# Kernel optimization log

Hardware: AMD Instinct MI355X
Metric: run time of the kernel (lower is better)

## Reference

```python
import jax, jax.numpy as jnp
import numpy as np
import math

NUM_HEADS = 16
HEAVY_RATIO = 0.1
RECENT_RATIO = 0.1
ROPE_THETA = 10000.0


def setup_inputs() -> dict:
    key = jax.random.key(0)
    ks = jax.random.split(key, 5)
    b, s, h = 1, 2048, 2048
    return {
        "hidden_states": jax.random.normal(ks[0], (b, s, h), dtype=jnp.float32),
        "Wq": jax.random.normal(ks[1], (h, h), dtype=jnp.float32) * 0.02,
        "Wk": jax.random.normal(ks[2], (h, h), dtype=jnp.float32) * 0.02,
        "Wv": jax.random.normal(ks[3], (h, h), dtype=jnp.float32) * 0.02,
        "Wo": jax.random.normal(ks[4], (h, h), dtype=jnp.float32) * 0.02,
    }


def _rotate_half(x):
    d = x.shape[-1]
    return jnp.concatenate([-x[..., d // 2:], x[..., : d // 2]], axis=-1)


def _rope(q, k, seq_len, head_dim, dtype):
    # LLaMA rotary embedding: inv_freq over even dims, emb = [freqs, freqs]
    inv_freq = 1.0 / (ROPE_THETA ** (jnp.arange(0, head_dim, 2, dtype=jnp.float32) / head_dim))
    pos = jnp.arange(seq_len, dtype=jnp.float32)
    freqs = pos[:, None] * inv_freq[None, :]            # [s, d/2]
    emb = jnp.concatenate([freqs, freqs], axis=-1)       # [s, d]
    cos = jnp.cos(emb).astype(dtype)[None, None]         # [1,1,s,d]
    sin = jnp.sin(emb).astype(dtype)[None, None]
    q = q * cos + _rotate_half(q) * sin
    k = k * cos + _rotate_half(k) * sin
    return q, k


def reference(hidden_states, Wq, Wk, Wv, Wo):
    b, s, hidden = hidden_states.shape
    H = NUM_HEADS
    d = hidden // H

    def proj(W):  # nn.Linear(x) = x @ W.T, then split heads -> [b,H,s,d]
        return (hidden_states @ W.T).reshape(b, s, H, d).transpose(0, 2, 1, 3)

    q, k, v = proj(Wq), proj(Wk), proj(Wv)
    q, k = _rope(q, k, s, d, hidden_states.dtype)

    scores = jnp.einsum("bhqd,bhkd->bhqk", q, k) / math.sqrt(d)  # [b,H,s,s]
    neg = jnp.finfo(scores.dtype).min
    i = jnp.arange(s)[:, None]
    j = jnp.arange(s)[None, :]
    causal = jnp.where(j <= i, jnp.array(0.0, scores.dtype), neg)
    scores = jnp.maximum(scores + causal, neg)

    heavy_budget = int(HEAVY_RATIO * s)
    recent_budget = int(RECENT_RATIO * s)

    # first softmax (fp32), accumulate column importances
    tmp_attn = jax.nn.softmax(scores.astype(jnp.float32), axis=-1).astype(scores.dtype)
    tmp_sum = jnp.sum(tmp_attn, axis=-2)                 # [b,H,s]
    _, topk_idx = jax.lax.top_k(tmp_sum, heavy_budget)   # [b,H,heavy]
    heavy_mask = jnp.any(topk_idx[..., :, None] == jnp.arange(s)[None, None, None, :], axis=-2)  # [b,H,s]

    # recent band: tril(diag=recent) & triu(diag=-recent)  <=>  |i-j| <= recent
    band = jnp.abs(i - j) <= recent_budget               # [s,s]
    mask = heavy_mask[:, :, None, :] | band[None, None]

    scores = jnp.where(mask, scores, neg)
    probs = jax.nn.softmax(scores.astype(jnp.float32), axis=-1).astype(q.dtype)
    attn = jnp.einsum("bhqk,bhkd->bhqd", probs, v)
    attn = attn.transpose(0, 2, 1, 3).reshape(b, s, hidden)
    return attn @ Wo.T
```

## Files before the change

### kernel.cpp

```cpp
#include <hip/hip_runtime.h>
#include <hip/hip_bf16.h>
#include <stdint.h>

#define SEQ   2048
#define HIDN  2048
#define NHEAD 16
#define HDIM  128
#define HEAVY 204
#define RECENT 204

typedef __attribute__((ext_vector_type(4))) float f32x4;
typedef __attribute__((ext_vector_type(8))) short bf16x8;
typedef unsigned short u16;
typedef unsigned int   u32;

static __device__ __forceinline__ u16 f2bf(float f){
  union { float f; u32 u; } v; v.f = f;
  u32 r = (v.u + 0x7FFFu + ((v.u >> 16) & 1u)) >> 16;
  return (u16)r;
}
static __device__ __forceinline__ float bf2f(u16 u){
  union { u32 u; float f; } v; v.u = ((u32)u) << 16;
  return v.f;
}

static __device__ __forceinline__ void gload16(const void* g, void* l){
  __builtin_amdgcn_global_load_lds((const __attribute__((address_space(1))) u32*)g,
                                   (__attribute__((address_space(3))) u32*)l, 16, 0, 0);
}

#define WAITVM(N) asm volatile("s_waitcnt vmcnt(" #N ")" ::: "memory")
#define BARRAW    __builtin_amdgcn_s_barrier()
#define PRIO1     __builtin_amdgcn_s_setprio(1)
#define PRIO0     __builtin_amdgcn_s_setprio(0)

static __device__ __forceinline__ void stage_tile(const u16* __restrict__ base, size_t stride,
                                                  int row0, u16* __restrict__ lds, int tid){
  const int wbase = tid & ~63;
#pragma unroll
  for (int it = 0; it < 4; ++it){
    int m = it * 256 + tid;
    int row = m >> 4, cp = m & 15;
    gload16(base + (size_t)(row0 + row) * stride + ((cp ^ (row & 7)) * 8),
            lds + (it * 256 + wbase) * 8);
  }
}

static __device__ __forceinline__ void stageK512(const u16* __restrict__ base, size_t stride,
                                                 int row0, u16* __restrict__ lds, int tid){
#pragma unroll
  for (int it = 0; it < 2; ++it){
    int m = it * 512 + tid;
    int row = m >> 4, cp = m & 15;
    gload16(base + (size_t)(row0 + row) * stride + ((cp ^ (row & 7)) * 8),
            lds + (it * 512 + (tid & ~63)) * 8);
  }
}
static __device__ __forceinline__ void stageV512(const u16* __restrict__ base, size_t stride,
                                                 int c0, u16* __restrict__ lds, int tid){
#pragma unroll
  for (int it = 0; it < 2; ++it){
    int m = it * 512 + tid;
    int row = m >> 3, cp = m & 7;
    gload16(base + (size_t)row * stride + c0 + ((cp ^ (row & 7)) * 8),
            lds + (it * 512 + (tid & ~63)) * 8);
  }
}

__global__ void k_prep(const float* __restrict__ A0, const float* __restrict__ A1,
                       const float* __restrict__ A2, const float* __restrict__ A3,
                       const float* __restrict__ A4, u16* __restrict__ out,
                       float* __restrict__ cosT, float* __restrict__ sinT,
                       float* __restrict__ colsum){
  int b = blockIdx.x, tid = threadIdx.x;
  if (b < 20480){
    int id = b * 256 + tid;
    int sel = id >> 20, off = (id & 1048575) * 4;
    const float* src = sel == 0 ? A0 : sel == 1 ? A1 : sel == 2 ? A2 : sel == 3 ? A3 : A4;
    float4 v = *(const float4*)(src + off);
    ushort4 o;
    o.x = f2bf(v.x); o.y = f2bf(v.y); o.z = f2bf(v.z); o.w = f2bf(v.w);
    *(ushort4*)(out + (size_t)sel * 4194304 + off) = o;
  } else if (b < 20992){
    int i = (b - 20480) * 256 + tid;
    int pos = i >> 6, j = i & 63;
    float invf = powf(10000.0f, -(float)j * (1.0f / 64.0f));
    float a = (float)pos * invf;
    cosT[i] = cosf(a);
    sinT[i] = sinf(a);
  } else {
    int i = (b - 20992) * 256 + tid;
    if (i < 16384) ((float4*)colsum)[i] = (float4){0.f, 0.f, 0.f, 0.f};
  }
}

__global__ void k_post(u16* __restrict__ Qm, u16* __restrict__ Km,
                       const float* __restrict__ cosT, const float* __restrict__ sinT,
                       const u16* __restrict__ V, u16* __restrict__ Vt){
  __shared__ u16 t[32][33];
  int b = blockIdx.x, tid = threadIdx.x;
  if (b < 4096){
    int gid = b * 256 + tid;
    u16* M = (gid < 524288) ? Qm : Km;
    int id = gid & 524287;
    int pos = id >> 8, rem = id & 255;
    int h = rem >> 4, j4 = (rem & 15) * 4;
    u16* p = M + (size_t)pos * HIDN + h * HDIM + j4;
    ushort4 lo = *(ushort4*)p;
    ushort4 hi = *(ushort4*)(p + 64);
    float4 c = *(const float4*)(cosT + pos * 64 + j4);
    float4 s = *(const float4*)(sinT + pos * 64 + j4);
    float l0 = bf2f(lo.x), l1 = bf2f(lo.y), l2 = bf2f(lo.z), l3 = bf2f(lo.w);
    float h0 = bf2f(hi.x), h1 = bf2f(hi.y), h2 = bf2f(hi.z), h3 = bf2f(hi.w);
    ushort4 nlo, nhi;
    nlo.x = f2bf(l0 * c.x - h0 * s.x);  nhi.x = f2bf(h0 * c.x + l0 * s.x);
    nlo.y = f2bf(l1 * c.y - h1 * s.y);  nhi.y = f2bf(h1 * c.y + l1 * s.y);
    nlo.z = f2bf(l2 * c.z - h2 * s.z);  nhi.z = f2bf(h2 * c.z + l2 * s.z);
    nlo.w = f2bf(l3 * c.w - h3 * s.w);  nhi.w = f2bf(h3 * c.w + l3 * s.w);
    *(ushort4*)p = nlo;
    *(ushort4*)(p + 64) = nhi;
  } else {
    int b2 = b - 4096;
    int s0 = (b2 & 63) * 32, c0 = (b2 >> 6) * 32;
    int r = tid >> 3, cc = (tid & 7) * 4;
    ushort4 v = *(const ushort4*)(V + (size_t)(s0 + r) * 2048 + c0 + cc);
    t[r][cc] = v.x; t[r][cc + 1] = v.y; t[r][cc + 2] = v.z; t[r][cc + 3] = v.w;
    __syncthreads();
    int co = tid >> 3, ro = (tid & 7) * 4;
    ushort4 o;
    o.x = t[ro][co]; o.y = t[ro + 1][co]; o.z = t[ro + 2][co]; o.w = t[ro + 3][co];
    *(ushort4*)(Vt + (size_t)(c0 + co) * 2048 + s0 + ro) = o;
  }
}

__global__ __launch_bounds__(512, 1)
void k_g256(const u16* __restrict__ X, const u16* __restrict__ Wq, const u16* __restrict__ Wk,
            const u16* __restrict__ Wv, u16* __restrict__ C0, u16* __restrict__ C1,
            u16* __restrict__ C2){
  __shared__ __align__(16) u16 LA[2][256 * 64];
  __shared__ __align__(16) u16 LB[2][192 * 64];
  const int tid = threadIdx.x;
  const int lane = tid & 63, wvi = tid >> 6;
  const int wm = wvi >> 2, wn = wvi & 3;
  const int g = lane >> 4, c15 = lane & 15;
  const int brow = blockIdx.y * 256;
  const int bcol = blockIdx.x * 192;
  const int NT = 32;

  f32x4 acc[8][3];
#pragma unroll
  for (int m = 0; m < 8; m++)
#pragma unroll
    for (int n = 0; n < 3; n++) acc[m][n] = (f32x4){0.f, 0.f, 0.f, 0.f};

  const int cc0 = ((g ^ (c15 & 7)) * 8);
  bf16x8 af[4][2], af2[4][2], bf[3][2];

#define BPTR(rB_) (rB_ < 2048 ? Wq + (size_t)(rB_) * 2048 \
                 : rB_ < 4096 ? Wk + (size_t)((rB_) - 2048) * 2048 \
                              : Wv + (size_t)((rB_) - 4096) * 2048)
#define STGA(grow0, gcol0, ldsb) do { \
  _Pragma("unroll") for (int it = 0; it < 2; ++it){ \
    int m_ = it * 512 + tid; \
    int row_ = m_ >> 3, cp_ = m_ & 7; \
    gload16(X + (size_t)((grow0) + row_) * 2048 + (gcol0) + ((cp_ ^ (row_ & 7)) * 8), \
            (ldsb) + (it * 512 + (tid & ~63)) * 8); \
  } } while(0)
#define STGB128(gcol0, ldsb) do { \
  _Pragma("unroll") for (int it = 0; it < 2; ++it){ \
    int m_ = it * 512 + tid; \
    int row_ = m_ >> 3, cp_ = m_ & 7; \
    int rB_ = bcol + row_; \
    const u16* bp_ = BPTR(rB_); \
    gload16(bp_ + (gcol0) + ((cp_ ^ (row_ & 7)) * 8), \
            (ldsb) + (it * 512 + (tid & ~63)) * 8); \
  } } while(0)
#define STGB64(gcol0, ldsb) do { \
    int row_ = 128 + (tid >> 3), cp_ = tid & 7; \
    int rB_ = bcol + row_; \
    const u16* bp_ = BPTR(rB_); \
    gload16(bp_ + (gcol0) + ((cp_ ^ (row_ & 7)) * 8), \
            (ldsb) + (tid & ~63) * 8); \
  } while(0)
#define RDA(buf) \
  _Pragma("unroll") for (int mi2 = 0; mi2 < 4; ++mi2){ \
    const u16* pr = &LA[buf][0] + (size_t)(wm * 128 + mi2 * 16 + c15) * 64; \
    af[mi2][0] = *(const bf16x8*)(pr + cc0); \
    af[mi2][1] = *(const bf16x8*)(pr + (cc0 ^ 32)); \
  }
#define RDA2(buf) \
  _Pragma("unroll") for (int mi2 = 0; mi2 < 4; ++mi2){ \
    const u16* pr = &LA[buf][0] + (size_t)(wm * 128 + (4 + mi2) * 16 + c15) * 64; \
    af2[mi2][0] = *(const bf16x8*)(pr + cc0); \
    af2[mi2][1] = *(const bf16x8*)(pr + (cc0 ^ 32)); \
  }
#define RDB2(buf) \
  _Pragma("unroll") for (int ni2 = 0; ni2 < 2; ++ni2){ \
    const u16* pr = &LB[buf][0] + (size_t)(wn * 48 + ni2 * 16 + c15) * 64; \
    bf[ni2][0] = *(const bf16x8*)(pr + cc0); \
    bf[ni2][1] = *(const bf16x8*)(pr + (cc0 ^ 32)); \
  }
#define RDB1(buf) do { \
    const u16* pr = &LB[buf][0] + (size_t)(wn * 48 + 32 + c15) * 64; \
    bf[2][0] = *(const bf16x8*)(pr + cc0); \
    bf[2][1] = *(const bf16x8*)(pr + (cc0 ^ 32)); \
  } while(0)
#define MM2A \
  _Pragma("unroll") for (int mi2 = 0; mi2 < 4; ++mi2) \
  _Pragma("unroll") for (int ni2 = 0; ni2 < 2; ++ni2) \
  _Pragma("unroll") for (int kk = 0; kk < 2; ++kk) \
    acc[mi2][ni2] = __builtin_amdgcn_mfma_f32_16x16x32_bf16( \
        af[mi2][kk], bf[ni2][kk], acc[mi2][ni2], 0, 0, 0);
#define MM1AB \
  _Pragma("unroll") for (int mi2 = 0; mi2 < 4; ++mi2) \
  _Pragma("unroll") for (int kk = 0; kk < 2; ++kk){ \
    acc[mi2][2] = __builtin_amdgcn_mfma_f32_16x16x32_bf16( \
        af[mi2][kk], bf[2][kk], acc[mi2][2], 0, 0, 0); \
    acc[4 + mi2][2] = __builtin_amdgcn_mfma_f32_16x16x32_bf16( \
        af2[mi2][kk], bf[2][kk], acc[4 + mi2][2], 0, 0, 0); \
  }
#define MM2B \
  _Pragma("unroll") for (int mi2 = 0; mi2 < 4; ++mi2) \
  _Pragma("unroll") for (int ni2 = 0; ni2 < 2; ++ni2) \
  _Pragma("unroll") for (int kk = 0; kk < 2; ++kk) \
    acc[4 + mi2][ni2] = __builtin_amdgcn_mfma_f32_16x16x32_bf16( \
        af2[mi2][kk], bf[ni2][kk], acc[4 + mi2][ni2], 0, 0, 0);

#define TILE(t, buf) do { \
    const int kn1 = ((t) + 1) * 64; \
    const int kn2 = ((t) + 2) * 64; \
     \
    RDA(buf); RDB2(buf); \
    if ((t) + 1 < NT) STGA(brow, kn1, &LA[buf ^ 1][0]); \
    BARRAW; PRIO1; MM2A; PRIO0; BARRAW; \
     \
    RDB1(buf); RDA2(buf); \
    if ((t) + 1 < NT) STGA(brow + 128, kn1, &LA[buf ^ 1][0] + 128 * 64); \
    BARRAW; PRIO1; MM1AB; PRIO0; BARRAW; \
     \
    if ((t) + 2 < NT){ STGB128(kn2, &LB[buf][0]); STGB64(kn2, &LB[buf][0] + 128 * 64); \
                       WAITVM(3); } \
    else             { WAITVM(0); } \
    BARRAW; PRIO1; MM2B; PRIO0; BARRAW; \
  } while(0)

  STGA(brow,       0, &LA[0][0]);
  STGA(brow + 128, 0, &LA[0][0] + 128 * 64);
  STGB128(0,  &LB[0][0]);
  STGB64(0,   &LB[0][0] + 128 * 64);
  STGB128(64, &LB[1][0]);
  STGB64(64,  &LB[1][0] + 128 * 64);
  WAITVM(3);
  BARRAW;

  for (int t = 0; t < NT; t += 2){
    TILE(t, 0);
    TILE(t + 1, 1);
  }
#undef TILE
#undef BPTR
#undef STGA
#undef STGB128
#undef STGB64
#undef RDA
#undef RDA2
#undef RDB2
#undef RDB1
#undef MM2A
#undef MM1AB
#undef MM2B

#pragma unroll
  for (int mi = 0; mi < 8; ++mi)
#pragma unroll
    for (int ni = 0; ni < 3; ++ni){
      int colbase = bcol + wn * 48 + ni * 16;
      int proj = colbase >> 11;
      u16* Cb = proj == 0 ? C0 : proj == 1 ? C1 : C2;
      int lc = (colbase & 2047) + c15;
#pragma unroll
      for (int r = 0; r < 4; ++r){
        int row = brow + wm * 128 + mi * 16 + g * 4 + r;
        Cb[(size_t)row * 2048 + lc] = f2bf(acc[mi][ni][r]);
      }
    }
}

__global__ __launch_bounds__(512)
void k_gemm_out(const u16* __restrict__ A, const u16* __restrict__ B, float* __restrict__ C){
  __shared__ __align__(16) u16 As[2][128 * 64];
  __shared__ __align__(16) u16 Bs[2][128 * 64];
  const int tid = threadIdx.x;
  const int w = tid >> 6, lane = tid & 63;
  const int wm = w >> 1, wn = w & 1;
  const int g = lane >> 4, c15 = lane & 15;
  const int brow = blockIdx.y * 128, bcol = blockIdx.x * 128;
  const int cc0 = ((g ^ (c15 & 7)) * 8);

  f32x4 acc[2][4];
#pragma unroll
  for (int m = 0; m < 2; m++)
#pragma unroll
    for (int n = 0; n < 4; n++) acc[m][n] = (f32x4){0.f, 0.f, 0.f, 0.f};

#define STG_O(k0, buf) do { \
  _Pragma("unroll") for (int it = 0; it < 2; ++it){ \
    int m_ = it * 512 + tid; \
    int row_ = m_ >> 3, cp_ = m_ & 7; \
    gload16(A + (size_t)(brow + row_) * 2048 + (k0) + ((cp_ ^ (row_ & 7)) * 8), \
            As[buf] + (it * 512 + (tid & ~63)) * 8); \
    gload16(B + (size_t)(bcol + row_) * 2048 + (k0) + ((cp_ ^ (row_ & 7)) * 8), \
            Bs[buf] + (it * 512 + (tid & ~63)) * 8); \
  } } while(0)

  STG_O(0, 0);
  int cur = 0;
  for (int kt = 0; kt < 32; ++kt){
    if (kt + 1 < 32){ STG_O((kt + 1) * 64, cur ^ 1); WAITVM(4); }
    else            { WAITVM(0); }
    BARRAW;
    bf16x8 af[2][2], bfr[4][2];
#pragma unroll
    for (int mi = 0; mi < 2; ++mi){
      const u16* pr = As[cur] + (size_t)(wm * 32 + mi * 16 + c15) * 64;
      af[mi][0] = *(const bf16x8*)(pr + cc0);
      af[mi][1] = *(const bf16x8*)(pr + (cc0 ^ 32));
    }
#pragma unroll
    for (int ni = 0; ni < 4; ++ni){
      const u16* pr = Bs[cur] + (size_t)(wn * 64 + ni * 16 + c15) * 64;
      bfr[ni][0] = *(const bf16x8*)(pr + cc0);
      bfr[ni][1] = *(const bf16x8*)(pr + (cc0 ^ 32));
    }
    PRIO1;
#pragma unroll
    for (int mi = 0; mi < 2; ++mi)
#pragma unroll
      for (int ni = 0; ni < 4; ++ni)
#pragma unroll
        for (int kk = 0; kk < 2; ++kk)
          acc[mi][ni] = __builtin_amdgcn_mfma_f32_16x16x32_bf16(af[mi][kk], bfr[ni][kk],
                                                                acc[mi][ni], 0, 0, 0);
    PRIO0;
    BARRAW;
    cur ^= 1;
  }
#undef STG_O
#pragma unroll
  for (int mi = 0; mi < 2; ++mi)
#pragma unroll
    for (int ni = 0; ni < 4; ++ni)
#pragma unroll
      for (int r = 0; r < 4; ++r){
        int row = brow + wm * 32 + mi * 16 + g * 4 + r;
        int col = bcol + wn * 64 + ni * 16 + c15;
        C[(size_t)row * 2048 + col] = acc[mi][ni][r];
      }
}

__global__ __launch_bounds__(256)
void k_pass1a(const u16* __restrict__ Q, const u16* __restrict__ K, float* __restrict__ rowsum){
  __shared__ __align__(16) u16 Ks[2][64 * 128];
  const int tid = threadIdx.x;
  const int wv = tid >> 6, lane = tid & 63;
  const int g = lane >> 4, c15 = lane & 15;
  const int h = blockIdx.y;
  int qb = 0, c = 0;
  { int rem = blockIdx.x; int q = 0;
    while (rem >= ((2 * q + 9) >> 3)){ rem -= (2 * q + 9) >> 3; q++; }
    qb = q; c = rem; }
  const int i0 = qb * 128;
  const int ktend = 2 * qb + 2;
  const int kt0 = c * 8;
  const int kt1 = (ktend < kt0 + 8) ? ktend : (kt0 + 8);
  const u16* Qh = Q + h * HDIM;
  const u16* Kh = K + h * HDIM;
  const float scale = 0.08838834764831845f;
  const int wb = wv * 32;

  bf16x8 qfr[2][4];
#pragma unroll
  for (int m = 0; m < 2; m++)
#pragma unroll
    for (int ks = 0; ks < 4; ks++)
      qfr[m][ks] = *(const bf16x8*)(Qh + (size_t)(i0 + wb + m * 16 + c15) * 2048 + ks * 32 + g * 8);

  stage_tile(Kh, 2048, kt0 * 64, Ks[0], tid);

  float rs[2][4] = {{0.f,0.f,0.f,0.f},{0.f,0.f,0.f,0.f}};
  int cur = 0;
  for (int kt = kt0; kt < kt1; ++kt){
    if (kt + 1 < kt1){ stage_tile(Kh, 2048, (kt + 1) * 64, Ks[cur ^ 1], tid); WAITVM(4); }
    else             { WAITVM(0); }
    BARRAW;
    const int k0 = kt * 64;
    f32x4 sacc[2][4];
#pragma unroll
    for (int m = 0; m < 2; m++)
#pragma unroll
      for (int n = 0; n < 4; n++) sacc[m][n] = (f32x4){0.f, 0.f, 0.f, 0.f};
#pragma unroll
    for (int ks = 0; ks < 4; ++ks){
#pragma unroll
      for (int n = 0; n < 4; n++){
        int brw = n * 16 + c15;
        bf16x8 b = *(const bf16x8*)(Ks[cur] + brw * 128 + ((ks * 32 + g * 8) ^ ((brw & 7) << 3)));
#pragma unroll
        for (int m = 0; m < 2; m++)
          sacc[m][n] = __builtin_amdgcn_mfma_f32_16x16x32_bf16(qfr[m][ks], b, sacc[m][n], 0, 0, 0);
      }
    }
    if (kt < 2 * qb){
#pragma unroll
      for (int m = 0; m < 2; m++)
#pragma unroll
        for (int n = 0; n < 4; n++)
#pragma unroll
          for (int r = 0; r < 4; r++)
            rs[m][r] += __expf(sacc[m][n][r] * scale);
    } else {
#pragma unroll
      for (int n = 0; n < 4; n++){
        int col = k0 + n * 16 + c15;
#pragma unroll
        for (int m = 0; m < 2; m++)
#pragma unroll
          for (int r = 0; r < 4; r++){
            int rowg = i0 + wb + m * 16 + g * 4 + r;
            rs[m][r] += (col <= rowg) ? __expf(sacc[m][n][r] * scale) : 0.f;
          }
      }
    }
    BARRAW;
    cur ^= 1;
  }
#pragma unroll
  for (int m = 0; m < 2; m++)
#pragma unroll
    for (int r = 0; r < 4; r++){
      float v = rs[m][r];
      v += __shfl_xor(v, 1); v += __shfl_xor(v, 2);
      v += __shfl_xor(v, 4); v += __shfl_xor(v, 8);
      if (c15 == 0)
        atomicAdd(&rowsum[h * 2048 + i0 + wb + m * 16 + g * 4 + r], v);
    }
}

__global__ __launch_bounds__(256)
void k_pass1b(const u16* __restrict__ Q, const u16* __restrict__ K,
              const float* __restrict__ rowsum, float* __restrict__ colsum){
  __shared__ __align__(16) u16 Qs[2][64 * 128];
  const int tid = threadIdx.x;
  const int wv = tid >> 6, lane = tid & 63;
  const int g = lane >> 4, c15 = lane & 15;
  const int h = blockIdx.y;
  int kb = 0, c = 0;
  { int rem = blockIdx.x; int q = 0;
    while (rem >= ((39 - 2 * q) >> 3)){ rem -= (39 - 2 * q) >> 3; q++; }
    kb = q; c = rem; }
  const int k0 = kb * 128;
  const int qt0 = 2 * kb + c * 8;
  const int qt1 = (2 * kb + c * 8 + 8 < 32) ? (2 * kb + c * 8 + 8) : 32;
  const u16* Qh = Q + h * HDIM;
  const u16* Kh = K + h * HDIM;
  const float scale = 0.08838834764831845f;
  const int wb = wv * 32;
  const float* rsrow = rowsum + h * 2048;

  bf16x8 kfr[2][4];
#pragma unroll
  for (int m = 0; m < 2; m++)
#pragma unroll
    for (int ks = 0; ks < 4; ks++)
      kfr[m][ks] = *(const bf16x8*)(Kh + (size_t)(k0 + wb + m * 16 + c15) * 2048 + ks * 32 + g * 8);

  stage_tile(Qh, 2048, qt0 * 64, Qs[0], tid);

  float racc[2][4] = {{0.f,0.f,0.f,0.f},{0.f,0.f,0.f,0.f}};
  int cur = 0;
  for (int qt = qt0; qt < qt1; ++qt){
    if (qt + 1 < qt1){ stage_tile(Qh, 2048, (qt + 1) * 64, Qs[cur ^ 1], tid); WAITVM(4); }
    else             { WAITVM(0); }
    BARRAW;
    const int i0q = qt * 64;
    float rw[4];
#pragma unroll
    for (int n = 0; n < 4; n++)
      rw[n] = 1.0f / rsrow[i0q + n * 16 + c15];
    f32x4 sacc[2][4];
#pragma unroll
    for (int m = 0; m < 2; m++)
#pragma unroll
      for (int n = 0; n < 4; n++) sacc[m][n] = (f32x4){0.f, 0.f, 0.f, 0.f};
#pragma unroll
    for (int ks = 0; ks < 4; ++ks){
#pragma unroll
      for (int n = 0; n < 4; n++){
        int brw = n * 16 + c15;
        bf16x8 b = *(const bf16x8*)(Qs[cur] + brw * 128 + ((ks * 32 + g * 8) ^ ((brw & 7) << 3)));
#pragma unroll
        for (int m = 0; m < 2; m++)
          sacc[m][n] = __builtin_amdgcn_mfma_f32_16x16x32_bf16(kfr[m][ks], b, sacc[m][n], 0, 0, 0);
      }
    }
    if (qt >= 2 * kb + 2){
#pragma unroll
      for (int m = 0; m < 2; m++)
#pragma unroll
        for (int n = 0; n < 4; n++)
#pragma unroll
          for (int r = 0; r < 4; r++)
            racc[m][r] += __expf(sacc[m][n][r] * scale) * rw[n];
    } else {
#pragma unroll
      for (int n = 0; n < 4; n++){
        int colq = i0q + n * 16 + c15;
#pragma unroll
        for (int m = 0; m < 2; m++)
#pragma unroll
          for (int r = 0; r < 4; r++){
            int rowk = k0 + wb + m * 16 + g * 4 + r;
            racc[m][r] += (rowk <= colq) ? __expf(sacc[m][n][r] * scale) * rw[n] : 0.f;
          }
      }
    }
    BARRAW;
    cur ^= 1;
  }
#pragma unroll
  for (int m = 0; m < 2; m++)
#pragma unroll
    for (int r = 0; r < 4; r++){
      float v = racc[m][r];
      v += __shfl_xor(v, 1); v += __shfl_xor(v, 2);
      v += __shfl_xor(v, 4); v += __shfl_xor(v, 8);
      if (c15 == 0)
        atomicAdd(&colsum[h * 2048 + k0 + wb + m * 16 + g * 4 + r], v);
    }
}

__global__ __launch_bounds__(1024)
void k_topk(const float* __restrict__ colsum, short* __restrict__ cidx){
  __shared__ u32 keys[2048];
  __shared__ int hist[256];
  __shared__ int chunkCnt[32];
  __shared__ short cidL[256];
  __shared__ u32 Tacc_s;
  __shared__ int rem_s;
  const int tid = threadIdx.x;
  const int h = blockIdx.x;
  const int w = tid >> 6, lane = tid & 63;

  for (int i = tid; i < 2048; i += 1024) keys[i] = ((const u32*)colsum)[h * 2048 + i];
  if (tid == 0){ Tacc_s = 0; rem_s = HEAVY; }
  __syncthreads();

  for (int s = 24; s >= 0; s -= 8){
    if (tid < 256) hist[tid] = 0;
    __syncthreads();
    u32 T = Tacc_s;
    for (int i = tid; i < 2048; i += 1024){
      u32 k = keys[i];
      bool match = (s == 24) ? true : (((k ^ T) >> (s + 8)) == 0);
      if (match) atomicAdd(&hist[(k >> s) & 255], 1);
    }
    __syncthreads();
    if (tid == 0){
      int rem = rem_s, acc = 0, b = 255;
      for (; b > 0; --b){
        int c2 = hist[b];
        if (acc + c2 >= rem) break;
        acc += c2;
      }
      Tacc_s = T | ((u32)b << s);
      rem_s = rem - acc;
    }
    __syncthreads();
  }
  const u32 T = Tacc_s;
  const int need = rem_s;
  const u32 kA = keys[tid], kB = keys[tid + 1024];
  const bool eqA = (kA == T), eqB = (kB == T);
  unsigned long long ebA = __ballot(eqA);
  unsigned long long ebB = __ballot(eqB);
  if (lane == 0){ chunkCnt[w] = __popcll(ebA); chunkCnt[16 + w] = __popcll(ebB); }
  __syncthreads();
  if (tid == 0){
    int s2 = 0;
    for (int i2 = 0; i2 < 32; ++i2){ int c2 = chunkCnt[i2]; chunkCnt[i2] = s2; s2 += c2; }
  }
  __syncthreads();
  const unsigned long long below = (1ull << lane) - 1ull;
  const int eqrA = chunkCnt[w] + __popcll(ebA & below);
  const int eqrB = chunkCnt[16 + w] + __popcll(ebB & below);
  const bool hvA = (kA > T) || (eqA && eqrA < need);
  const bool hvB = (kB > T) || (eqB && eqrB < need);
  __syncthreads();
  unsigned long long hbA = __ballot(hvA);
  unsigned long long hbB = __ballot(hvB);
  if (lane == 0){ chunkCnt[w] = __popcll(hbA); chunkCnt[16 + w] = __popcll(hbB); }
  if (tid >= HEAVY && tid < 256) cidL[tid] = 32767;
  __syncthreads();
  if (tid == 0){
    int s2 = 0;
    for (int i2 = 0; i2 < 32; ++i2){ int c2 = chunkCnt[i2]; chunkCnt[i2] = s2; s2 += c2; }
  }
  __syncthreads();
  if (hvA) cidL[chunkCnt[w] + __popcll(hbA & below)] = (short)tid;
  if (hvB) cidL[chunkCnt[16 + w] + __popcll(hbB & below)] = (short)(tid + 1024);
  __syncthreads();
  if (tid < 256) cidx[h * 256 + tid] = cidL[tid];
}

__global__ void k_gath(const u16* __restrict__ Kb, const u16* __restrict__ Vb,
                       const short* __restrict__ cidx,
                       u16* __restrict__ Kg, u16* __restrict__ Vg){
  __shared__ __align__(16) u16 t[32][136];
  int b = blockIdx.x, tid = threadIdx.x;
  if (b < 256){
    int gid = b * 256 + tid;
    int h = gid >> 12, rem = gid & 4095;
    int slot = rem >> 4, cp = rem & 15;
    int cid = cidx[h * 256 + slot];
    bf16x8 z = (bf16x8){0,0,0,0,0,0,0,0};
    bf16x8 val = (cid < 2048) ? *(const bf16x8*)(Kb + (size_t)cid * 2048 + h * 128 + cp * 8) : z;
    *(bf16x8*)(Kg + ((size_t)h * 256 + slot) * 128 + cp * 8) = val;
  } else {
    int b2 = b - 256;
    int h = b2 >> 3, s0 = (b2 & 7) * 32;
#pragma unroll
    for (int it = 0; it < 2; ++it){
      int m = it * 256 + tid;
      int s = m >> 4, cp = m & 15;
      int cid = cidx[h * 256 + s0 + s];
      bf16x8 z = (bf16x8){0,0,0,0,0,0,0,0};
      bf16x8 val = (cid < 2048) ? *(const bf16x8*)(Vb + (size_t)cid * 2048 + h * 128 + cp * 8) : z;
      *(bf16x8*)(&t[s][cp * 8]) = val;
    }
    __syncthreads();
#pragma unroll
    for (int i = 0; i < 16; ++i){
      int idx = i * 256 + tid;
      int d = idx >> 5, s = idx & 31;
      Vg[((size_t)h * 128 + d) * 256 + s0 + s] = t[s][d];
    }
  }
}

__global__ __launch_bounds__(512)
void k_pass2(const u16* __restrict__ Q, const u16* __restrict__ K, const u16* __restrict__ Vt,
             const u16* __restrict__ Kg, const u16* __restrict__ Vg,
             const short* __restrict__ cidx, u16* __restrict__ attn){
  __shared__ __align__(16) u16 Ks[2][64 * 128];
  __shared__ __align__(16) u16 Vs[2][128 * 64];
  __shared__ __align__(16) u16 Ps[8][16 * 64];
  __shared__ short cids[256];
  __shared__ int lists[12];
  __shared__ int nact_s;
  const int tid = threadIdx.x;
  const int w = tid >> 6, lane = tid & 63;
  const int g = lane >> 4, c15 = lane & 15;
  const int qb = blockIdx.x, h = blockIdx.y;
  const int i0 = qb * 128;
  const int wq = w >> 2, w4 = w & 3;
  const int rowbase = i0 + wq * 64 + w4 * 16;
  const u16* Qh = Q + h * HDIM;
  const u16* Kh = K + h * HDIM;
  const u16* Kgh = Kg + (size_t)h * 256 * 128;
  const u16* Vth = Vt + (size_t)h * 128 * 2048;
  const u16* Vgh = Vg + (size_t)h * 128 * 256;
  const float scale = 0.08838834764831845f;

  if (tid < 256) cids[tid] = cidx[h * 256 + tid];
  bf16x8 qfr[4];
#pragma unroll
  for (int ks = 0; ks < 4; ks++)
    qfr[ks] = *(const bf16x8*)(Qh + (size_t)(rowbase + c15) * 2048 + ks * 32 + g * 8);
  __syncthreads();
  if (tid == 0){
    int n = 0;
    int ktb0 = (i0 > RECENT) ? ((i0 - RECENT) >> 6) : 0;
    int ktmax = (i0 + 127) >> 6;
    for (int kt = ktb0; kt <= ktmax; ++kt) lists[n++] = kt;
    for (int gt = 0; gt < 4; ++gt)
      if ((int)cids[gt * 64] <= i0 + 127 - RECENT - 1) lists[n++] = 100 + gt;
    nact_s = n;
  }
  __syncthreads();
  const int nact = nact_s;

  { int e = lists[0];
    if (e < 100){ stageK512(Kh, 2048, e * 64, Ks[0], tid);
                  stageV512(Vth, 2048, e * 64, Vs[0], tid); }
    else        { stageK512(Kgh, 128, (e - 100) * 64, Ks[0], tid);
                  stageV512(Vgh, 256, (e - 100) * 64, Vs[0], tid); } }
  WAITVM(2);
  BARRAW;

  f32x4 oacc[8];
#pragma unroll
  for (int f = 0; f < 8; f++) oacc[f] = (f32x4){0.f, 0.f, 0.f, 0.f};
  float lsum[4] = {0.f, 0.f, 0.f, 0.f};

  int cur = 0;
  for (int i = 0; i < nact; ++i){
    const int e = lists[i];
    const bool isg = (e >= 100);
    const bool nxt = (i + 1 < nact);
    if (nxt){
      int e2 = lists[i + 1];
      if (e2 < 100){ stageK512(Kh, 2048, e2 * 64, Ks[cur ^ 1], tid);
                     stageV512(Vth, 2048, e2 * 64, Vs[cur ^ 1], tid); }
      else         { stageK512(Kgh, 128, (e2 - 100) * 64, Ks[cur ^ 1], tid);
                     stageV512(Vgh, 256, (e2 - 100) * 64, Vs[cur ^ 1], tid); }
      WAITVM(6);
    } else {
      WAITVM(2);
    }
    BARRAW;
    f32x4 sacc[4];
#pragma unroll
    for (int n = 0; n < 4; n++) sacc[n] = (f32x4){0.f, 0.f, 0.f, 0.f};
#pragma unroll
    for (int ks = 0; ks < 4; ++ks){
#pragma unroll
      for (int n = 0; n < 4; n++){
        int brw = n * 16 + c15;
        bf16x8 b = *(const bf16x8*)(Ks[cur] + brw * 128 + ((ks * 32 + g * 8) ^ ((brw & 7) << 3)));
        sacc[n] = __builtin_amdgcn_mfma_f32_16x16x32_bf16(qfr[ks], b, sacc[n], 0, 0, 0);
      }
    }
#pragma unroll
    for (int n = 0; n < 4; n++){
      int cid = isg ? (int)cids[(e - 100) * 64 + n * 16 + c15] : (e * 64 + n * 16 + c15);
#pragma unroll
      for (int r = 0; r < 4; r++){
        int rowg = rowbase + g * 4 + r;
        int dist = rowg - cid;
        bool valid = (cid <= rowg) && (isg ? (dist > RECENT) : (dist <= RECENT));
        float ev = valid ? __expf(sacc[n][r] * scale) : 0.f;
        lsum[r] += ev;
        int prow = g * 4 + r;
        Ps[w][prow * 64 + ((n * 16 + c15) ^ ((prow & 7) << 3))] = f2bf(ev);
      }
    }
    if (nxt) WAITVM(4); else WAITVM(0);
    BARRAW;
    PRIO1;
#pragma unroll
    for (int ks2 = 0; ks2 < 2; ++ks2){
      bf16x8 pa = *(const bf16x8*)(&Ps[w][c15 * 64 + ((ks2 * 32 + g * 8) ^ ((c15 & 7) << 3))]);
#pragma unroll
      for (int f = 0; f < 8; ++f){
        int vrow = f * 16 + c15;
        bf16x8 vb = *(const bf16x8*)(Vs[cur] + vrow * 64 + ((ks2 * 32 + g * 8) ^ ((vrow & 7) << 3)));
        oacc[f] = __builtin_amdgcn_mfma_f32_16x16x32_bf16(pa, vb, oacc[f], 0, 0, 0);
      }
    }
    PRIO0;
    BARRAW;
    cur ^= 1;
  }
  float rinv[4];
#pragma unroll
  for (int r = 0; r < 4; r++){
    float v = lsum[r];
    v += __shfl_xor(v, 1); v += __shfl_xor(v, 2);
    v += __shfl_xor(v, 4); v += __shfl_xor(v, 8);
    rinv[r] = 1.0f / v;
  }
#pragma unroll
  for (int f = 0; f < 8; f++)
#pragma unroll
    for (int r = 0; r < 4; r++){
      int rowg = rowbase + g * 4 + r;
      attn[(size_t)rowg * 2048 + h * HDIM + f * 16 + c15] = f2bf(oacc[f][r] * rinv[r]);
    }
}

extern "C" void kernel_launch(void* const* d_in, const int* in_sizes, int n_in,
                              void* d_out, int out_size, void* d_ws, size_t ws_size,
                              hipStream_t stream){
  const float* X  = (const float*)d_in[0];
  const float* Wq = (const float*)d_in[1];
  const float* Wk = (const float*)d_in[2];
  const float* Wv = (const float*)d_in[3];
  const float* Wo = (const float*)d_in[4];

  char* w = (char*)d_ws;
  const size_t MB8 = (size_t)2048 * 2048 * 2;
  u16* Xb  = (u16*)(w);
  u16* Wqb = (u16*)(w + 1 * MB8);
  u16* Wkb = (u16*)(w + 2 * MB8);
  u16* Wvb = (u16*)(w + 3 * MB8);
  u16* Wob = (u16*)(w + 4 * MB8);
  u16* Qb  = (u16*)(w + 5 * MB8);
  u16* Kb  = (u16*)(w + 6 * MB8);
  u16* Vb  = (u16*)(w + 7 * MB8);
  u16* Vtb   = Wqb;
  u16* attnb = Xb;
  char* p = w + 8 * MB8;
  float* cosT = (float*)p;              p += 524288;
  float* sinT = (float*)p;              p += 524288;
  float* colsum = (float*)p;            p += 131072;
  float* rowsum = (float*)p;            p += 131072;
  short* cidx  = (short*)p;             p += 16 * 256 * 2;
  u16*   Kg    = (u16*)p;               p += (size_t)16 * 256 * 128 * 2;
  u16*   Vg    = (u16*)p;

  dim3 b256(256);

  k_prep<<<21056, b256, 0, stream>>>(X, Wq, Wk, Wv, Wo, Xb, cosT, sinT, colsum);

  k_g256<<<dim3(32, 8), dim3(512), 0, stream>>>(Xb, Wqb, Wkb, Wvb, Qb, Kb, Vb);
  k_post<<<8192, b256, 0, stream>>>(Qb, Kb, cosT, sinT, Vb, Vtb);

  k_pass1a<<<dim3(40, 16), b256, 0, stream>>>(Qb, Kb, rowsum);
  k_pass1b<<<dim3(40, 16), b256, 0, stream>>>(Qb, Kb, rowsum, colsum);
  k_topk<<<16, dim3(1024), 0, stream>>>(colsum, cidx);
  k_gath<<<384, b256, 0, stream>>>(Kb, Vb, cidx, Kg, Vg);
  k_pass2<<<dim3(16, 16), dim3(512), 0, stream>>>(Qb, Kb, Vtb, Kg, Vg, cidx, attnb);

  k_gemm_out<<<dim3(16, 16), dim3(512), 0, stream>>>(attnb, Wob, (float*)d_out);
}
```

Measured before the change: 243.0 us.

## Triple-buffer score passes and cut barriers in GEMM and attention pipelines

The GEMM tile macro merges its first two compute phases, issues both A-half prefetches up front, and drops several barriers. The row-sum and column-sum passes move from double to triple LDS buffering, so the prefetch two tiles ahead is issued after the barrier and the trailing barrier is removed. The sparse attention loop moves its wait and barrier to the top of the iteration and drops the trailing barrier. The aim is fewer workgroup barriers and more overlap of global loads with MFMA work, at the cost of extra LDS (which may lower occupancy) and a risk of hazards from removed barriers.

```diff
diff --git a/kernel.cpp b/kernel.cpp
--- a/kernel.cpp
+++ b/kernel.cpp
@@ -229,19 +229,16 @@
 #define TILE(t, buf) do { \
     const int kn1 = ((t) + 1) * 64; \
     const int kn2 = ((t) + 2) * 64; \
-     \
-    RDA(buf); RDB2(buf); \
-    if ((t) + 1 < NT) STGA(brow, kn1, &LA[buf ^ 1][0]); \
-    BARRAW; PRIO1; MM2A; PRIO0; BARRAW; \
-     \
-    RDB1(buf); RDA2(buf); \
-    if ((t) + 1 < NT) STGA(brow + 128, kn1, &LA[buf ^ 1][0] + 128 * 64); \
-    BARRAW; PRIO1; MM1AB; PRIO0; BARRAW; \
-     \
-    if ((t) + 2 < NT){ STGB128(kn2, &LB[buf][0]); STGB64(kn2, &LB[buf][0] + 128 * 64); \
-                       WAITVM(3); } \
-    else             { WAITVM(0); } \
-    BARRAW; PRIO1; MM2B; PRIO0; BARRAW; \
+    RDA(buf); RDB2(buf); RDA2(buf); RDB1(buf); \
+    if ((t) + 1 < NT){ STGA(brow, kn1, &LA[buf ^ 1][0]); \
+                       STGA(brow + 128, kn1, &LA[buf ^ 1][0] + 128 * 64); } \
+    PRIO1; MM2A; MM1AB; PRIO0; \
+    BARRAW; \
+    if ((t) + 2 < NT){ STGB128(kn2, &LB[buf][0]); STGB64(kn2, &LB[buf][0] + 128 * 64); } \
+    PRIO1; MM2B; PRIO0; \
+    if ((t) + 2 < NT){ WAITVM(3); } \
+    else if ((t) + 1 < NT){ WAITVM(0); } \
+    BARRAW; \
   } while(0)
 
   STGA(brow,       0, &LA[0][0]);
@@ -360,7 +357,7 @@
 
 __global__ __launch_bounds__(256)
 void k_pass1a(const u16* __restrict__ Q, const u16* __restrict__ K, float* __restrict__ rowsum){
-  __shared__ __align__(16) u16 Ks[2][64 * 128];
+  __shared__ __align__(16) u16 Ks[3][64 * 128];
   const int tid = threadIdx.x;
   const int wv = tid >> 6, lane = tid & 63;
   const int g = lane >> 4, c15 = lane & 15;
@@ -386,13 +383,14 @@
       qfr[m][ks] = *(const bf16x8*)(Qh + (size_t)(i0 + wb + m * 16 + c15) * 2048 + ks * 32 + g * 8);
 
   stage_tile(Kh, 2048, kt0 * 64, Ks[0], tid);
+  if (kt0 + 1 < kt1) stage_tile(Kh, 2048, (kt0 + 1) * 64, Ks[1], tid);
 
   float rs[2][4] = {{0.f,0.f,0.f,0.f},{0.f,0.f,0.f,0.f}};
-  int cur = 0;
   for (int kt = kt0; kt < kt1; ++kt){
-    if (kt + 1 < kt1){ stage_tile(Kh, 2048, (kt + 1) * 64, Ks[cur ^ 1], tid); WAITVM(4); }
-    else             { WAITVM(0); }
+    const int bi = (kt - kt0) % 3;
+    if (kt + 1 < kt1){ WAITVM(4); } else { WAITVM(0); }
     BARRAW;
+    if (kt + 2 < kt1) stage_tile(Kh, 2048, (kt + 2) * 64, Ks[(kt - kt0 + 2) % 3], tid);
     const int k0 = kt * 64;
     f32x4 sacc[2][4];
 #pragma unroll
@@ -404,7 +402,7 @@
 #pragma unroll
       for (int n = 0; n < 4; n++){
         int brw = n * 16 + c15;
-        bf16x8 b = *(const bf16x8*)(Ks[cur] + brw * 128 + ((ks * 32 + g * 8) ^ ((brw & 7) << 3)));
+        bf16x8 b = *(const bf16x8*)(Ks[bi] + brw * 128 + ((ks * 32 + g * 8) ^ ((brw & 7) << 3)));
 #pragma unroll
         for (int m = 0; m < 2; m++)
           sacc[m][n] = __builtin_amdgcn_mfma_f32_16x16x32_bf16(qfr[m][ks], b, sacc[m][n], 0, 0, 0);
@@ -431,8 +429,6 @@
           }
       }
     }
-    BARRAW;
-    cur ^= 1;
   }
 #pragma unroll
   for (int m = 0; m < 2; m++)
@@ -449,7 +445,7 @@
 __global__ __launch_bounds__(256)
 void k_pass1b(const u16* __restrict__ Q, const u16* __restrict__ K,
               const float* __restrict__ rowsum, float* __restrict__ colsum){
-  __shared__ __align__(16) u16 Qs[2][64 * 128];
+  __shared__ __align__(16) u16 Qs[3][64 * 128];
   const int tid = threadIdx.x;
   const int wv = tid >> 6, lane = tid & 63;
   const int g = lane >> 4, c15 = lane & 15;
@@ -475,13 +471,14 @@
       kfr[m][ks] = *(const bf16x8*)(Kh + (size_t)(k0 + wb + m * 16 + c15) * 2048 + ks * 32 + g * 8);
 
   stage_tile(Qh, 2048, qt0 * 64, Qs[0], tid);
+  if (qt0 + 1 < qt1) stage_tile(Qh, 2048, (qt0 + 1) * 64, Qs[1], tid);
 
   float racc[2][4] = {{0.f,0.f,0.f,0.f},{0.f,0.f,0.f,0.f}};
-  int cur = 0;
   for (int qt = qt0; qt < qt1; ++qt){
-    if (qt + 1 < qt1){ stage_tile(Qh, 2048, (qt + 1) * 64, Qs[cur ^ 1], tid); WAITVM(4); }
-    else             { WAITVM(0); }
+    const int bi = (qt - qt0) % 3;
+    if (qt + 1 < qt1){ WAITVM(4); } else { WAITVM(0); }
     BARRAW;
+    if (qt + 2 < qt1) stage_tile(Qh, 2048, (qt + 2) * 64, Qs[(qt - qt0 + 2) % 3], tid);
     const int i0q = qt * 64;
     float rw[4];
 #pragma unroll
@@ -497,7 +494,7 @@
 #pragma unroll
       for (int n = 0; n < 4; n++){
         int brw = n * 16 + c15;
-        bf16x8 b = *(const bf16x8*)(Qs[cur] + brw * 128 + ((ks * 32 + g * 8) ^ ((brw & 7) << 3)));
+        bf16x8 b = *(const bf16x8*)(Qs[bi] + brw * 128 + ((ks * 32 + g * 8) ^ ((brw & 7) << 3)));
 #pragma unroll
         for (int m = 0; m < 2; m++)
           sacc[m][n] = __builtin_amdgcn_mfma_f32_16x16x32_bf16(kfr[m][ks], b, sacc[m][n], 0, 0, 0);
@@ -524,8 +521,6 @@
           }
       }
     }
-    BARRAW;
-    cur ^= 1;
   }
 #pragma unroll
   for (int m = 0; m < 2; m++)
@@ -694,8 +689,6 @@
                   stageV512(Vth, 2048, e * 64, Vs[0], tid); }
     else        { stageK512(Kgh, 128, (e - 100) * 64, Ks[0], tid);
                   stageV512(Vgh, 256, (e - 100) * 64, Vs[0], tid); } }
-  WAITVM(2);
-  BARRAW;
 
   f32x4 oacc[8];
 #pragma unroll
@@ -707,17 +700,15 @@
     const int e = lists[i];
     const bool isg = (e >= 100);
     const bool nxt = (i + 1 < nact);
+    WAITVM(2);
+    BARRAW;
     if (nxt){
       int e2 = lists[i + 1];
       if (e2 < 100){ stageK512(Kh, 2048, e2 * 64, Ks[cur ^ 1], tid);
                      stageV512(Vth, 2048, e2 * 64, Vs[cur ^ 1], tid); }
       else         { stageK512(Kgh, 128, (e2 - 100) * 64, Ks[cur ^ 1], tid);
                      stageV512(Vgh, 256, (e2 - 100) * 64, Vs[cur ^ 1], tid); }
-      WAITVM(6);
-    } else {
-      WAITVM(2);
-    }
-    BARRAW;
+    }
     f32x4 sacc[4];
 #pragma unroll
     for (int n = 0; n < 4; n++) sacc[n] = (f32x4){0.f, 0.f, 0.f, 0.f};
@@ -758,7 +749,6 @@
       }
     }
     PRIO0;
-    BARRAW;
     cur ^= 1;
   }
   float rinv[4];
```

Measured after the change: 239.1 us, median of 2. No clear change (-1.6%).
